# Optimization experiments

Hardware: AMD Instinct MI355X
Metric: run time of the kernel (lower is better)

The kernel has to match this reference:

```python
import jax, jax.numpy as jnp
import numpy as np

H, C, G = 4, 32, 64          # heads, per-head channels, num graphs
D_IN, HID = 128, 128          # input feature dim, dueling MLP hidden
NEG_SLOPE = 0.2               # GATv2Conv default negative_slope


def setup_inputs() -> dict:
    key = jax.random.key(0)
    ks = jax.random.split(key, 16)
    N, E = 50000, 800000
    x = jax.random.normal(ks[0], (N, D_IN), jnp.float32)
    edge_index = jax.random.randint(ks[1], (2, E), 0, N, dtype=jnp.int64)
    batch = jnp.sort(jax.random.randint(ks[2], (N,), 0, G, dtype=jnp.int64))
    s_in = 1.0 / np.sqrt(D_IN)
    s_g = 1.0 / np.sqrt(H * C)
    s_h = 1.0 / np.sqrt(HID)
    return {
        "x": x,
        "W_l": jax.random.normal(ks[3], (D_IN, H * C), jnp.float32) * s_in,
        "b_l": jnp.zeros((H * C,), jnp.float32),
        "W_r": jax.random.normal(ks[4], (D_IN, H * C), jnp.float32) * s_in,
        "b_r": jnp.zeros((H * C,), jnp.float32),
        "att": jax.random.normal(ks[5], (H, C), jnp.float32) * (1.0 / np.sqrt(C)),
        "bias": jnp.zeros((H * C,), jnp.float32),
        "Wq1": jax.random.normal(ks[6], (H * C, HID), jnp.float32) * s_g,
        "bq1": jnp.zeros((HID,), jnp.float32),
        "Wq2": jax.random.normal(ks[7], (HID, 2), jnp.float32) * s_h,
        "bq2": jnp.zeros((2,), jnp.float32),
        "Wv1": jax.random.normal(ks[8], (H * C, HID), jnp.float32) * s_g,
        "bv1": jnp.zeros((HID,), jnp.float32),
        "Wv2": jax.random.normal(ks[9], (HID, 1), jnp.float32) * s_h,
        "bv2": jnp.zeros((1,), jnp.float32),
        "edge_index": edge_index,
        "batch": batch,
    }


def reference(x, W_l, b_l, W_r, b_r, att, bias,
              Wq1, bq1, Wq2, bq2, Wv1, bv1, Wv2, bv2,
              edge_index, batch):
    N = x.shape[0]
    # add self loops (PyG GATv2Conv default)
    loop = jnp.arange(N, dtype=edge_index.dtype)
    src = jnp.concatenate([edge_index[0], loop])  # message source j
    dst = jnp.concatenate([edge_index[1], loop])  # aggregation target i

    xl = (x @ W_l + b_l).reshape(N, H, C)  # source transform
    xr = (x @ W_r + b_r).reshape(N, H, C)  # target transform

    # per-edge GATv2 score: a^T LeakyReLU(xl_j + xr_i), shape [Et, H]
    m = jax.nn.leaky_relu(xl[src] + xr[dst], NEG_SLOPE)
    e = jnp.einsum('ehc,hc->eh', m, att)

    # segment softmax over incoming edges of each target node
    emax = jax.ops.segment_max(e, dst, num_segments=N)
    ee = jnp.exp(e - emax[dst])
    denom = jax.ops.segment_sum(ee, dst, num_segments=N)
    alpha = ee / (denom[dst] + 1e-16)  # [Et, H]

    # scatter-add weighted source features, concat heads
    out = jax.ops.segment_sum(alpha[:, :, None] * xl[src], dst, num_segments=N)
    h = jax.nn.relu(out.reshape(N, H * C) + bias)

    # global max pool per graph
    g = jax.ops.segment_max(h, batch, num_segments=G)  # [G, H*C]

    # dueling heads
    q = jax.nn.relu(g @ Wq1 + bq1) @ Wq2 + bq2  # [G, 2]
    v = jax.nn.relu(g @ Wv1 + bv1) @ Wv2 + bv2  # [G, 1]
    return q - q.mean(axis=1, keepdims=True) + v
```

## Files before the change

kernel.cpp:

```cpp
#include <hip/hip_runtime.h>
#include <hip/hip_fp16.h>

#define F   128
#define DIN 128
#define HID 128
#define NEG 0.2f
#define L2E 1.4426950408889634f
#define KNODE 8
#define CAP  64

typedef _Float16 hvec2 __attribute__((ext_vector_type(2)));
typedef _Float16 half8 __attribute__((ext_vector_type(8)));
typedef float f32x4 __attribute__((ext_vector_type(4)));
union U2 { unsigned u; hvec2 v; };
union UH { _Float16 f; unsigned short u; };

template<int CTRL>
__device__ __forceinline__ float dpp_addf(float x){
    int t = __builtin_amdgcn_update_dpp(0, __float_as_int(x), CTRL, 0xF, 0xF, true);
    return x + __int_as_float(t);
}

__global__ void k_prep(const float* __restrict__ Wl, const float* __restrict__ Wr,
                       const float* __restrict__ att,
                       const float* __restrict__ bl, const float* __restrict__ br,
                       unsigned short* __restrict__ WT, unsigned* __restrict__ att_h,
                       float* __restrict__ bcat, unsigned* __restrict__ zbase, int nz,
                       int* __restrict__ slots, int N){
    const int e = blockIdx.x * 256 + threadIdx.x;
    if (e < 32768){
        const int k = e >> 8, col = e & 255;
        const float w = (col < 128) ? Wl[k * 128 + col] : Wr[k * 128 + (col - 128)];
        UH u; u.f = (_Float16)w;
        WT[col * 128 + k] = u.u;
    }
    if (e < 64){
        float2 a2 = ((const float2*)att)[e];
        U2 r; r.v = hvec2{(_Float16)(a2.x * L2E), (_Float16)(a2.y * L2E)};
        att_h[e] = r.u;
    }
    if (e < 256) bcat[e] = (e < 128) ? bl[e] : br[e - 128];
    if (e < nz) zbase[e] = 0u;
    if (e < N)  slots[(size_t)e << 6] = e;
}

__global__ __launch_bounds__(256) void k_mm(const float* __restrict__ x,
                      const unsigned short* __restrict__ WT, const float* __restrict__ bcat,
                      unsigned short* __restrict__ xl_s, unsigned short* __restrict__ xr_s,
                      int N){
    const int t = threadIdx.x;
    const int w = t >> 6, lane = t & 63;
    const int li = lane & 15, hi = lane >> 4;
    const int rowA = blockIdx.x * 64 + w * 16 + li;
    const int rA = (rowA < N) ? rowA : N - 1;
    f32x4 acc[16];
    #pragma unroll
    for (int c = 0; c < 16; ++c) acc[c] = f32x4{0.f, 0.f, 0.f, 0.f};
    #pragma unroll
    for (int kt = 0; kt < 4; ++kt){
        const int k0 = kt * 32 + hi * 8;
        const float4 f0 = *(const float4*)(x + (size_t)rA * DIN + k0);
        const float4 f1 = *(const float4*)(x + (size_t)rA * DIN + k0 + 4);
        half8 b;
        b[0] = (_Float16)f0.x; b[1] = (_Float16)f0.y; b[2] = (_Float16)f0.z; b[3] = (_Float16)f0.w;
        b[4] = (_Float16)f1.x; b[5] = (_Float16)f1.y; b[6] = (_Float16)f1.z; b[7] = (_Float16)f1.w;
        #pragma unroll
        for (int c = 0; c < 16; ++c){
            const half8 a = *(const half8*)(WT + (size_t)(c * 16 + li) * 128 + k0);
            acc[c] = __builtin_amdgcn_mfma_f32_16x16x32_f16(a, b, acc[c], 0, 0, 0);
        }
    }
    if (rowA < N){
        #pragma unroll
        for (int c = 0; c < 16; ++c){
            const int col0 = c * 16 + hi * 4;
            const float4 bv = *(const float4*)(bcat + col0);
            UH p0, p1, p2, p3;
            p0.f = (_Float16)(acc[c][0] + bv.x);
            p1.f = (_Float16)(acc[c][1] + bv.y);
            p2.f = (_Float16)(acc[c][2] + bv.z);
            p3.f = (_Float16)(acc[c][3] + bv.w);
            uint2 val;
            val.x = (unsigned)p0.u | ((unsigned)p1.u << 16);
            val.y = (unsigned)p2.u | ((unsigned)p3.u << 16);
            if (col0 < 128) *(uint2*)(xl_s + (size_t)rowA * F + col0)         = val;
            else            *(uint2*)(xr_s + (size_t)rowA * F + (col0 - 128)) = val;
        }
    }
}

__global__ void k_scatter(const int* __restrict__ ei, unsigned* __restrict__ cnt,
                          int* __restrict__ slots, int E){
    int t = blockIdx.x * blockDim.x + threadIdx.x;
    if (t >= E) return;
    const int dst = ei[E + t];
    const unsigned pos = atomicAdd(&cnt[dst], 1u);
    if (pos < CAP - 1) slots[((size_t)dst << 6) + 1 + pos] = ei[t];
}

__global__ void k_node(const unsigned* __restrict__ xl_h, const unsigned* __restrict__ xr_h,
                       const int* __restrict__ slots, const unsigned* __restrict__ cnt,
                       const unsigned* __restrict__ att_h, const float* __restrict__ bias,
                       const int* __restrict__ batch, unsigned* __restrict__ g_bits, int N){
    const int wid  = (int)(((long long)blockIdx.x * blockDim.x + threadIdx.x) >> 6);
    const int lane = threadIdx.x & 63;
    const int i0 = wid * KNODE;
    if (i0 >= N) return;
    U2 atv; atv.u = att_h[lane];
    const float2 bz = ((const float2*)bias)[lane];
    const hvec2 neg2 = {(_Float16)NEG, (_Float16)NEG};
    float pool0 = 0.f, pool1 = 0.f;
    int curg = __builtin_amdgcn_readfirstlane(batch[i0]);
    const int iend = (i0 + KNODE < N) ? i0 + KNODE : N;

    for (int i = i0; i < iend; ++i){
        const int g = __builtin_amdgcn_readfirstlane(batch[i]);
        if (g != curg){
            atomicMax(&g_bits[curg * F + 2 * lane],     __float_as_uint(pool0));
            atomicMax(&g_bits[curg * F + 2 * lane + 1], __float_as_uint(pool1));
            pool0 = 0.f; pool1 = 0.f; curg = g;
        }
        const int rs = i << 6;
        int dt = (int)cnt[i] + 1;
        if (dt > CAP) dt = CAP;
        U2 xrv; xrv.u = xr_h[(size_t)i * 64 + lane];

        float d0=0.f,d1=0.f,d2=0.f,d3=0.f,d4=0.f,d5=0.f,d6=0.f,d7=0.f;
        float ax0=0.f,ax1=0.f,ax2=0.f,ax3=0.f,ax4=0.f,ax5=0.f,ax6=0.f,ax7=0.f;
        float ay0=0.f,ay1=0.f,ay2=0.f,ay3=0.f,ay4=0.f,ay5=0.f,ay6=0.f,ay7=0.f;

        auto proc = [&](unsigned hv, float& d_, float& ax_, float& ay_){
            U2 xlv; xlv.u = hv;
            hvec2 z = xlv.v + xrv.v;
            hvec2 r = __builtin_elementwise_max(z, z * neg2);
#if __has_builtin(__builtin_amdgcn_fdot2)
            float s = __builtin_amdgcn_fdot2(r, atv.v, 0.f, false);
#else
            float s = fmaf((float)r.x, (float)atv.v.x, (float)r.y * (float)atv.v.y);
#endif
            s = dpp_addf<0xB1>(s);
            s = dpp_addf<0x4E>(s);
            s = dpp_addf<0x124>(s);
            s = dpp_addf<0x128>(s);
            const float p = exp2f(s);
            d_ += p;
            ax_ = fmaf(p, (float)xlv.v.x, ax_);
            ay_ = fmaf(p, (float)xlv.v.y, ay_);
        };

        const int my_src = (lane < dt) ? slots[rs + lane] : i;
        int e = 0;
        for (; e + 7 < dt; e += 8){
            const int s0 = __builtin_amdgcn_readlane(my_src, e);
            const int s1 = __builtin_amdgcn_readlane(my_src, e + 1);
            const int s2 = __builtin_amdgcn_readlane(my_src, e + 2);
            const int s3 = __builtin_amdgcn_readlane(my_src, e + 3);
            const int s4 = __builtin_amdgcn_readlane(my_src, e + 4);
            const int s5 = __builtin_amdgcn_readlane(my_src, e + 5);
            const int s6 = __builtin_amdgcn_readlane(my_src, e + 6);
            const int s7 = __builtin_amdgcn_readlane(my_src, e + 7);
            const unsigned h0 = xl_h[(size_t)s0 * 64 + lane];
            const unsigned h1 = xl_h[(size_t)s1 * 64 + lane];
            const unsigned h2 = xl_h[(size_t)s2 * 64 + lane];
            const unsigned h3 = xl_h[(size_t)s3 * 64 + lane];
            const unsigned h4 = xl_h[(size_t)s4 * 64 + lane];
            const unsigned h5 = xl_h[(size_t)s5 * 64 + lane];
            const unsigned h6 = xl_h[(size_t)s6 * 64 + lane];
            const unsigned h7 = xl_h[(size_t)s7 * 64 + lane];
            proc(h0, d0, ax0, ay0); proc(h1, d1, ax1, ay1);
            proc(h2, d2, ax2, ay2); proc(h3, d3, ax3, ay3);
            proc(h4, d4, ax4, ay4); proc(h5, d5, ax5, ay5);
            proc(h6, d6, ax6, ay6); proc(h7, d7, ax7, ay7);
        }
        for (; e + 3 < dt; e += 4){
            const int s0 = __builtin_amdgcn_readlane(my_src, e);
            const int s1 = __builtin_amdgcn_readlane(my_src, e + 1);
            const int s2 = __builtin_amdgcn_readlane(my_src, e + 2);
            const int s3 = __builtin_amdgcn_readlane(my_src, e + 3);
            const unsigned h0 = xl_h[(size_t)s0 * 64 + lane];
            const unsigned h1 = xl_h[(size_t)s1 * 64 + lane];
            const unsigned h2 = xl_h[(size_t)s2 * 64 + lane];
            const unsigned h3 = xl_h[(size_t)s3 * 64 + lane];
            proc(h0, d0, ax0, ay0); proc(h1, d1, ax1, ay1);
            proc(h2, d2, ax2, ay2); proc(h3, d3, ax3, ay3);
        }
        for (; e < dt; ++e){
            const int s0 = __builtin_amdgcn_readlane(my_src, e);
            proc(xl_h[(size_t)s0 * 64 + lane], d0, ax0, ay0);
        }

        const float dsum = ((d0 + d1) + (d2 + d3)) + ((d4 + d5) + (d6 + d7));
        const float ax = ((ax0 + ax1) + (ax2 + ax3)) + ((ax4 + ax5) + (ax6 + ax7));
        const float ay = ((ay0 + ay1) + (ay2 + ay3)) + ((ay4 + ay5) + (ay6 + ay7));
        const float inv = 1.f / (dsum + 1e-16f);
        pool0 = fmaxf(pool0, fmaxf(fmaf(ax, inv, bz.x), 0.f));
        pool1 = fmaxf(pool1, fmaxf(fmaf(ay, inv, bz.y), 0.f));
    }
    atomicMax(&g_bits[curg * F + 2 * lane],     __float_as_uint(pool0));
    atomicMax(&g_bits[curg * F + 2 * lane + 1], __float_as_uint(pool1));
}

__global__ void k_dueling(const float* __restrict__ g,
                          const float* __restrict__ Wq1, const float* __restrict__ bq1,
                          const float* __restrict__ Wq2, const float* __restrict__ bq2,
                          const float* __restrict__ Wv1, const float* __restrict__ bv1,
                          const float* __restrict__ Wv2, const float* __restrict__ bv2,
                          float* __restrict__ out){
    __shared__ float gs[F], red0[128], red1[128], red2[128];
    const int t = threadIdx.x, gi = blockIdx.x;
    gs[t] = g[gi * F + t];
    __syncthreads();
    float aq = bq1[t], av = bv1[t];
    for (int k = 0; k < F; ++k){
        aq = fmaf(gs[k], Wq1[k * HID + t], aq);
        av = fmaf(gs[k], Wv1[k * HID + t], av);
    }
    aq = aq > 0.f ? aq : 0.f;
    av = av > 0.f ? av : 0.f;
    red0[t] = aq * Wq2[t * 2 + 0];
    red1[t] = aq * Wq2[t * 2 + 1];
    red2[t] = av * Wv2[t];
    __syncthreads();
    for (int off = 64; off > 0; off >>= 1){
        if (t < off){ red0[t] += red0[t + off]; red1[t] += red1[t + off]; red2[t] += red2[t + off]; }
        __syncthreads();
    }
    if (t == 0){
        const float q0 = red0[0] + bq2[0];
        const float q1 = red1[0] + bq2[1];
        const float v  = red2[0] + bv2[0];
        out[gi * 2 + 0] = 0.5f * (q0 - q1) + v;
        out[gi * 2 + 1] = 0.5f * (q1 - q0) + v;
    }
}

extern "C" void kernel_launch(void* const* d_in, const int* in_sizes, int n_in,
                              void* d_out, int out_size, void* d_ws, size_t ws_size,
                              hipStream_t stream) {
    const float* x    = (const float*)d_in[0];
    const float* Wl   = (const float*)d_in[1];
    const float* bl   = (const float*)d_in[2];
    const float* Wr   = (const float*)d_in[3];
    const float* br   = (const float*)d_in[4];
    const float* att  = (const float*)d_in[5];
    const float* bias = (const float*)d_in[6];
    const float* Wq1  = (const float*)d_in[7];
    const float* bq1  = (const float*)d_in[8];
    const float* Wq2  = (const float*)d_in[9];
    const float* bq2  = (const float*)d_in[10];
    const float* Wv1  = (const float*)d_in[11];
    const float* bv1  = (const float*)d_in[12];
    const float* Wv2  = (const float*)d_in[13];
    const float* bv2  = (const float*)d_in[14];
    const int*   ei   = (const int*)d_in[15];
    const int*   batch= (const int*)d_in[16];
    float* out = (float*)d_out;

    const int N  = in_sizes[0] / DIN;
    const int E  = in_sizes[15] / 2;
    const int Gg = out_size / 2;
    const int GF = Gg * F;

    unsigned* xl_h   = (unsigned*)d_ws;
    unsigned* xr_h   = xl_h + (size_t)N * 64;
    unsigned* att_h  = xr_h + (size_t)N * 64;
    unsigned* WT     = att_h + 64;
    float*    bcat   = (float*)(WT + 16384);
    unsigned* cnt    = (unsigned*)(bcat + 256);
    unsigned* g_bits = cnt + N;
    int*      slots  = (int*)(g_bits + GF);

    const int NZ = N + GF;
    int mx = 32768; if (N > mx) mx = N; if (NZ > mx) mx = NZ;
    const int prep_blocks = (mx + 255) / 256;

    k_prep<<<prep_blocks, 256, 0, stream>>>(Wl, Wr, att, bl, br, (unsigned short*)WT,
                                            att_h, bcat, cnt, NZ, slots, N);
    k_scatter<<<(E + 255) / 256, 256, 0, stream>>>(ei, cnt, slots, E);
    k_mm<<<(N + 63) / 64, 256, 0, stream>>>(x, (const unsigned short*)WT, bcat,
                                            (unsigned short*)xl_h, (unsigned short*)xr_h, N);
    {
        const long long waves = (N + KNODE - 1) / KNODE;
        const long long thr = waves * 64;
        k_node<<<(unsigned)((thr + 255) / 256), 256, 0, stream>>>(
            xl_h, xr_h, slots, cnt, att_h, bias, batch, g_bits, N);
    }
    k_dueling<<<Gg, 128, 0, stream>>>((const float*)g_bits, Wq1, bq1, Wq2, bq2,
                                      Wv1, bv1, Wv2, bv2, out);
}
```

Baseline: 165.8 us.

## Fuse edge scatter and projection matmul into one heterogeneous launch

```diff
diff --git a/kernel.cpp b/kernel.cpp
--- a/kernel.cpp
+++ b/kernel.cpp
@@ -25,8 +25,7 @@
                        const float* __restrict__ att,
                        const float* __restrict__ bl, const float* __restrict__ br,
                        unsigned short* __restrict__ WT, unsigned* __restrict__ att_h,
-                       float* __restrict__ bcat, unsigned* __restrict__ zbase, int nz,
-                       int* __restrict__ slots, int N){
+                       float* __restrict__ bcat){
     const int e = blockIdx.x * 256 + threadIdx.x;
     if (e < 32768){
         const int k = e >> 8, col = e & 255;
@@ -40,18 +39,41 @@
         att_h[e] = r.u;
     }
     if (e < 256) bcat[e] = (e < 128) ? bl[e] : br[e - 128];
-    if (e < nz) zbase[e] = 0u;
-    if (e < N)  slots[(size_t)e << 6] = e;
-}
-
-__global__ __launch_bounds__(256) void k_mm(const float* __restrict__ x,
-                      const unsigned short* __restrict__ WT, const float* __restrict__ bcat,
-                      unsigned short* __restrict__ xl_s, unsigned short* __restrict__ xr_s,
-                      int N){
+}
+
+__global__ __launch_bounds__(256) void k_fused(
+        const float* __restrict__ x, const unsigned short* __restrict__ WT,
+        const float* __restrict__ bcat,
+        unsigned short* __restrict__ xl_s, unsigned short* __restrict__ xr_s, int N,
+        const int* __restrict__ ei, unsigned* __restrict__ cnt,
+        int* __restrict__ slots, int E, int SCB){
+    if ((int)blockIdx.x < SCB){
+        const int base = ((int)blockIdx.x * 256 + threadIdx.x) * 4;
+        if (base >= E) return;
+        int s0, s1, s2, s3, d0, d1, d2, d3;
+        if (base + 3 < E && ((E & 3) == 0)){
+            const int4 sv = *(const int4*)(ei + base);
+            const int4 dv = *(const int4*)(ei + E + base);
+            s0 = sv.x; s1 = sv.y; s2 = sv.z; s3 = sv.w;
+            d0 = dv.x; d1 = dv.y; d2 = dv.z; d3 = dv.w;
+        } else {
+            s0 = ei[base]; d0 = ei[E + base];
+            s1 = (base+1 < E) ? ei[base+1] : 0; d1 = (base+1 < E) ? ei[E+base+1] : -1;
+            s2 = (base+2 < E) ? ei[base+2] : 0; d2 = (base+2 < E) ? ei[E+base+2] : -1;
+            s3 = (base+3 < E) ? ei[base+3] : 0; d3 = (base+3 < E) ? ei[E+base+3] : -1;
+        }
+        unsigned p;
+        if (d0 >= 0){ p = atomicAdd(&cnt[d0], 1u); if (p < CAP-1) slots[((size_t)d0 << 6) + 1 + p] = s0; }
+        if (d1 >= 0){ p = atomicAdd(&cnt[d1], 1u); if (p < CAP-1) slots[((size_t)d1 << 6) + 1 + p] = s1; }
+        if (d2 >= 0){ p = atomicAdd(&cnt[d2], 1u); if (p < CAP-1) slots[((size_t)d2 << 6) + 1 + p] = s2; }
+        if (d3 >= 0){ p = atomicAdd(&cnt[d3], 1u); if (p < CAP-1) slots[((size_t)d3 << 6) + 1 + p] = s3; }
+        return;
+    }
+    const int mb = (int)blockIdx.x - SCB;
     const int t = threadIdx.x;
     const int w = t >> 6, lane = t & 63;
     const int li = lane & 15, hi = lane >> 4;
-    const int rowA = blockIdx.x * 64 + w * 16 + li;
+    const int rowA = mb * 64 + w * 16 + li;
     const int rA = (rowA < N) ? rowA : N - 1;
     f32x4 acc[16];
     #pragma unroll
@@ -87,15 +109,6 @@
             else            *(uint2*)(xr_s + (size_t)rowA * F + (col0 - 128)) = val;
         }
     }
-}
-
-__global__ void k_scatter(const int* __restrict__ ei, unsigned* __restrict__ cnt,
-                          int* __restrict__ slots, int E){
-    int t = blockIdx.x * blockDim.x + threadIdx.x;
-    if (t >= E) return;
-    const int dst = ei[E + t];
-    const unsigned pos = atomicAdd(&cnt[dst], 1u);
-    if (pos < CAP - 1) slots[((size_t)dst << 6) + 1 + pos] = ei[t];
 }
 
 __global__ void k_node(const unsigned* __restrict__ xl_h, const unsigned* __restrict__ xr_h,
@@ -148,7 +161,7 @@
             ay_ = fmaf(p, (float)xlv.v.y, ay_);
         };
 
-        const int my_src = (lane < dt) ? slots[rs + lane] : i;
+        const int my_src = (lane > 0 && lane < dt) ? slots[rs + lane] : i;
         int e = 0;
         for (; e + 7 < dt; e += 8){
             const int s0 = __builtin_amdgcn_readlane(my_src, e);
@@ -270,15 +283,14 @@
     unsigned* g_bits = cnt + N;
     int*      slots  = (int*)(g_bits + GF);
 
-    const int NZ = N + GF;
-    int mx = 32768; if (N > mx) mx = N; if (NZ > mx) mx = NZ;
-    const int prep_blocks = (mx + 255) / 256;
-
-    k_prep<<<prep_blocks, 256, 0, stream>>>(Wl, Wr, att, bl, br, (unsigned short*)WT,
-                                            att_h, bcat, cnt, NZ, slots, N);
-    k_scatter<<<(E + 255) / 256, 256, 0, stream>>>(ei, cnt, slots, E);
-    k_mm<<<(N + 63) / 64, 256, 0, stream>>>(x, (const unsigned short*)WT, bcat,
-                                            (unsigned short*)xl_h, (unsigned short*)xr_h, N);
+    const int SCB = (E + 1023) / 1024;
+    const int MMB = (N + 63) / 64;
+
+    (void)hipMemsetAsync(cnt, 0, (size_t)(N + GF) * sizeof(unsigned), stream);
+    k_prep<<<128, 256, 0, stream>>>(Wl, Wr, att, bl, br, (unsigned short*)WT, att_h, bcat);
+    k_fused<<<SCB + MMB, 256, 0, stream>>>(x, (const unsigned short*)WT, bcat,
+                                           (unsigned short*)xl_h, (unsigned short*)xr_h, N,
+                                           ei, cnt, slots, E, SCB);
     {
         const long long waves = (N + KNODE - 1) / KNODE;
         const long long thr = waves * 64;
```

Measured after the change: 163.7 us. About the same (-1.2%).
